# Kernel optimization log

Hardware: AMD Instinct MI355X
Metric: run time of the kernel (lower is better)

Reference implementation:

```python
import jax, jax.numpy as jnp
import numpy as np

N_E = 1024
E_DIM = 64
BETA = 0.25


def setup_inputs() -> dict:
    key = jax.random.key(0)
    k1, k2 = jax.random.split(key)
    z = jax.random.normal(k1, (16, E_DIM, 64, 64), dtype=jnp.float32)
    # embedding initialized uniform(-1/n_e, 1/n_e) as in the torch module
    emb = jax.random.uniform(k2, (N_E, E_DIM), dtype=jnp.float32,
                             minval=-1.0 / N_E, maxval=1.0 / N_E)
    return {"z": z, "emb": emb}


def reference(z, emb):
    n_e, e_dim = emb.shape
    # NCHW -> NHWC, flatten to tokens
    zp = jnp.transpose(z, (0, 2, 3, 1))            # [B,H,W,C]
    zf = zp.reshape(-1, e_dim)                      # [N,C]
    # squared distances ||zf||^2 + ||e||^2 - 2 zf e^T  -> [N, n_e]
    d = (jnp.sum(zf * zf, axis=1, keepdims=True)
         + jnp.sum(emb * emb, axis=1)
         - 2.0 * jnp.matmul(zf, emb.T))
    idx = jnp.argmin(d, axis=1)                     # [N]
    # one-hot @ emb is exactly a gather
    z_q = emb[idx].reshape(zp.shape)                # [B,H,W,C]
    loss = (jnp.mean((jax.lax.stop_gradient(z_q) - zp) ** 2)
            + BETA * jnp.mean((z_q - jax.lax.stop_gradient(zp)) ** 2))
    # straight-through estimator
    z_q = zp + jax.lax.stop_gradient(z_q - zp)
    # perplexity from codeword usage histogram
    counts = jax.ops.segment_sum(jnp.ones_like(idx, dtype=zf.dtype), idx,
                                 num_segments=n_e)
    e_mean = counts / zf.shape[0]
    perplexity = jnp.exp(-jnp.sum(e_mean * jnp.log(e_mean + 1e-10)))
    min_encoding_indices = idx.reshape(z.shape[0], -1).astype(jnp.int32)
    z_q = jnp.transpose(z_q, (0, 3, 1, 2))          # back to NCHW
    return z_q, loss, perplexity, min_encoding_indices
```

## Files before the change

### kernel.cpp

```cpp
#include <hip/hip_runtime.h>

#define TOKS 65536
#define ED 64
#define NE 1024
#define CH_STRIDE 4096
#define B_STRIDE 262144

typedef __bf16 bf16x8 __attribute__((ext_vector_type(8)));
typedef float f32x16 __attribute__((ext_vector_type(16)));
typedef unsigned short ushort_t;
typedef unsigned int uint_t;


__device__ __forceinline__ ushort_t f2bf(float x) {
    uint_t u = __float_as_uint(x);
    uint_t r = u + 0x7FFFu + ((u >> 16) & 1u);
    return (ushort_t)(r >> 16);
}

__global__ __launch_bounds__(256) void vq_prep_e(const float* __restrict__ emb,
                                                 ushort_t* __restrict__ efrag,
                                                 float* __restrict__ enorm,
                                                 int* __restrict__ hist,
                                                 double* __restrict__ lossAcc) {
    const int tid = threadIdx.x;
    const int w = tid >> 6, lane = tid & 63;
    const int j = blockIdx.x * 4 + w;

    const float e = emb[j * 64 + lane];
    const float sq = __fmul_rn(e, e);
    float acc = sq;
    acc = __fadd_rn(acc, __shfl_down(sq, 8, 64));
    acc = __fadd_rn(acc, __shfl_down(sq, 16, 64));
    acc = __fadd_rn(acc, __shfl_down(sq, 24, 64));
    acc = __fadd_rn(acc, __shfl_down(sq, 32, 64));
    acc = __fadd_rn(acc, __shfl_down(sq, 40, 64));
    acc = __fadd_rn(acc, __shfl_down(sq, 48, 64));
    acc = __fadd_rn(acc, __shfl_down(sq, 56, 64));
    float x = __fadd_rn(acc, __shfl_down(acc, 1, 64));
    float y = __fadd_rn(x, __shfl_down(x, 2, 64));
    float zn = __fadd_rn(y, __shfl_down(y, 4, 64));
    if (lane == 0) enorm[j] = zn;

    const ushort_t h = f2bf(-2.0f * e);
    const int ct = j >> 5, m = j & 31;
    const int ks = lane >> 4, kh = (lane >> 3) & 1, i = lane & 7;
    efrag[(size_t)((ct * 4 + ks) * 512) + (m + 32 * kh) * 8 + i] = h;

    if (blockIdx.x < 4) hist[blockIdx.x * 256 + tid] = 0;
    if (blockIdx.x == 0 && tid == 0) *lossAcc = 0.0;
}

__global__ __launch_bounds__(256, 4) void vq_main(
    const float* __restrict__ z,
    const ushort_t* __restrict__ efrag,
    const float* __restrict__ enorm,
    const float* __restrict__ emb,
    float* __restrict__ zq,
    float* __restrict__ out_idx,
    int* __restrict__ hist,
    double* __restrict__ lossAcc) {
    __shared__ float z_s[64][36];
    __shared__ uint_t skey[4][32][2][3];
    __shared__ float s_zn[32];
    __shared__ unsigned long long s_res[32];
    __shared__ uint_t s_cand[128];
    __shared__ int s_cnt;
    __shared__ double wsum[4];

    const int tid = threadIdx.x;
    const int w = tid >> 6, lane = tid & 63;
    const int t0 = blockIdx.x * 32;
    const int b = t0 >> 12, hw0 = t0 & 4095;
    const float* zbase = z + (size_t)b * B_STRIDE + hw0;

    {
        const int c = tid >> 2, u0 = (tid & 3) * 8;
        const float* src = zbase + (size_t)c * CH_STRIDE + u0;
        float4 f0 = *(const float4*)(src);
        float4 f1 = *(const float4*)(src + 4);
        *(float4*)&z_s[c][u0] = f0;
        *(float4*)&z_s[c][u0 + 4] = f1;
    }
    if (tid < 32) s_res[tid] = 0xFFFFFFFFFFFFFFFFull;
    if (tid == 0) s_cnt = 0;

    const int n = lane & 31, kh = lane >> 5;

    bf16x8 zb[4];
    #pragma unroll
    for (int ks = 0; ks < 4; ++ks) {
        #pragma unroll
        for (int i = 0; i < 8; ++i) {
            union { ushort_t u; __bf16 bh; } ca;
            ca.u = f2bf(zbase[(size_t)(ks * 16 + kh * 8 + i) * CH_STRIDE + n]);
            zb[ks][i] = ca.bh;
        }
    }

    uint_t k0 = 0xFFFFFFFFu, k1 = 0xFFFFFFFFu, k2 = 0xFFFFFFFFu;
    const bf16x8* eg = (const bf16x8*)efrag;

    #pragma unroll
    for (int ct = 0; ct < 8; ++ct) {
        const int gct = w * 8 + ct;
        bf16x8 ah0 = eg[(size_t)(gct * 4 + 0) * 64 + lane];
        bf16x8 ah1 = eg[(size_t)(gct * 4 + 1) * 64 + lane];
        bf16x8 ah2 = eg[(size_t)(gct * 4 + 2) * 64 + lane];
        bf16x8 ah3 = eg[(size_t)(gct * 4 + 3) * 64 + lane];

        f32x16 acc;
        #pragma unroll
        for (int r = 0; r < 16; ++r) acc[r] = 0.25f;
        acc = __builtin_amdgcn_mfma_f32_32x32x16_bf16(ah0, zb[0], acc, 0, 0, 0);
        acc = __builtin_amdgcn_mfma_f32_32x32x16_bf16(ah1, zb[1], acc, 0, 0, 0);
        acc = __builtin_amdgcn_mfma_f32_32x32x16_bf16(ah2, zb[2], acc, 0, 0, 0);
        acc = __builtin_amdgcn_mfma_f32_32x32x16_bf16(ah3, zb[3], acc, 0, 0, 0);

        const int jb = gct * 32 + 4 * kh;
        #pragma unroll
        for (int r = 0; r < 16; ++r) {
            uint_t key = (__float_as_uint(acc[r]) & 0xFFFFFC00u)
                         | (uint_t)(jb + (r & 3) + 8 * (r >> 2));
            uint_t mx = max(k0, key);
            k2 = min(k2, max(k1, mx));
            k1 = min(k1, mx);
            k0 = min(k0, key);
        }
    }

    skey[w][n][kh][0] = k0; skey[w][n][kh][1] = k1; skey[w][n][kh][2] = k2;
    __syncthreads();

    const int t_loc = tid >> 3, m = tid & 7;
    {
        float a = z_s[m][t_loc];
        float racc = __fmul_rn(a, a);
        #pragma unroll
        for (int i = 1; i < 8; ++i) {
            float av = z_s[m + 8 * i][t_loc];
            racc = __fadd_rn(racc, __fmul_rn(av, av));
        }
        float x1 = __fadd_rn(racc, __shfl_xor(racc, 1, 64));
        float y1 = __fadd_rn(x1, __shfl_xor(x1, 2, 64));
        float zn = __fadd_rn(y1, __shfl_xor(y1, 4, 64));
        if (m == 0) s_zn[t_loc] = zn;
    }
    {
        uint_t ck[3];
        #pragma unroll
        for (int s = 0; s < 3; ++s) ck[s] = skey[m >> 1][t_loc][m & 1][s];
        uint_t kmin = min(ck[0], min(ck[1], ck[2]));
        kmin = min(kmin, (uint_t)__shfl_xor((int)kmin, 1, 64));
        kmin = min(kmin, (uint_t)__shfl_xor((int)kmin, 2, 64));
        kmin = min(kmin, (uint_t)__shfl_xor((int)kmin, 4, 64));
        const float thr = __uint_as_float(kmin & 0xFFFFFC00u) + 4.0e-4f;
        #pragma unroll
        for (int s = 0; s < 3; ++s) {
            if (__uint_as_float(ck[s] & 0xFFFFFC00u) <= thr) {
                int pos = atomicAdd(&s_cnt, 1);
                if (pos < 128)
                    s_cand[pos] = ((uint_t)t_loc << 10) | (ck[s] & 1023u);
            }
        }
    }
    __syncthreads();

    {
        const int cnt = s_cnt;
        if (tid < cnt && tid < 128) {
            const uint_t cd = s_cand[tid];
            const int tok = (int)(cd >> 10), j = (int)(cd & 1023u);
            const float* e = emb + (size_t)j * 64;
            float a0 = 0.f;
            #pragma unroll
            for (int k4 = 0; k4 < 64; k4 += 4) {
                float4 e4 = *(const float4*)(e + k4);
                a0 = __fmaf_rn(z_s[k4 + 0][tok], e4.x, a0);
                a0 = __fmaf_rn(z_s[k4 + 1][tok], e4.y, a0);
                a0 = __fmaf_rn(z_s[k4 + 2][tok], e4.z, a0);
                a0 = __fmaf_rn(z_s[k4 + 3][tok], e4.w, a0);
            }
            float d = __fsub_rn(__fadd_rn(s_zn[tok], enorm[j]), 2.0f * a0);
            unsigned long long key =
                ((unsigned long long)__float_as_uint(d) << 10)
                | (unsigned long long)j;
            atomicMin(&s_res[tok], key);
        }
    }
    __syncthreads();

    const int bj = (int)(s_res[t_loc] & 1023u);
    if (m == 0) {
        out_idx[t0 + t_loc] = (float)bj;
        atomicAdd(&hist[bj], 1);
    }
    double ls = 0.0;
    {
        const float* e = emb + (size_t)bj * 64;
        #pragma unroll
        for (int i = 0; i < 8; ++i) {
            const int k = m + 8 * i;
            float ev = e[k];
            float zv = z_s[k][t_loc];
            z_s[k][t_loc] = ev;
            float df = ev - zv;
            ls += (double)(df * df);
        }
    }
    #pragma unroll
    for (int off = 32; off > 0; off >>= 1) ls += __shfl_down(ls, off, 64);
    if (lane == 0) wsum[w] = ls;
    __syncthreads();
    if (tid == 0)
        atomicAdd(lossAcc, wsum[0] + wsum[1] + wsum[2] + wsum[3]);

    {
        const int c = tid >> 2, u0 = (tid & 3) * 8;
        float4 f0 = *(const float4*)&z_s[c][u0];
        float4 f1 = *(const float4*)&z_s[c][u0 + 4];
        float* dst = zq + (size_t)b * B_STRIDE + (size_t)c * CH_STRIDE + hw0 + u0;
        *(float4*)(dst) = f0;
        *(float4*)(dst + 4) = f1;
    }
}

__global__ __launch_bounds__(256) void vq_final(const int* __restrict__ hist,
                                                const double* __restrict__ lossAcc,
                                                float* __restrict__ outs) {
    __shared__ double red[256];
    double acc = 0.0;
    for (int j = threadIdx.x; j < NE; j += 256) {
        double em = (double)hist[j] * (1.0 / 65536.0);
        acc += em * log(em + 1e-10);
    }
    red[threadIdx.x] = acc;
    __syncthreads();
    for (int s = 128; s > 0; s >>= 1) {
        if (threadIdx.x < s) red[threadIdx.x] += red[threadIdx.x + s];
        __syncthreads();
    }
    if (threadIdx.x == 0) {
        outs[0] = (float)(1.25 * (*lossAcc) * (1.0 / 4194304.0));
        outs[1] = (float)exp(-red[0]);
    }
}

extern "C" void kernel_launch(void* const* d_in, const int* in_sizes, int n_in,
                              void* d_out, int out_size, void* d_ws, size_t ws_size,
                              hipStream_t stream) {
    const float* z = (const float*)d_in[0];
    const float* emb = (const float*)d_in[1];
    float* out = (float*)d_out;

    char* ws = (char*)d_ws;
    ushort_t* efrag = (ushort_t*)ws;
    float* enorm = (float*)(ws + 131072);
    int* hist = (int*)(ws + 135168);
    double* lossAcc = (double*)(ws + 139264);

    float* zq = out;
    float* scalars = out + 4194304;
    float* out_idx = out + 4194306;

    vq_prep_e<<<256, 256, 0, stream>>>(emb, efrag, enorm, hist, lossAcc);
    vq_main<<<2048, 256, 0, stream>>>(z, efrag, enorm, emb, zq, out_idx, hist, lossAcc);
    vq_final<<<1, 256, 0, stream>>>(hist, lossAcc, scalars);
}
```

Before: 49.23 us.

## Replace top-3 key tracking with two-pass min-threshold candidate selection

The old code kept a sorted top-3 key per lane. The new code runs the MFMA distance tiles twice: the first pass finds only the per-token approximate minimum, and the second pass recomputes the tiles and collects every codeword within the threshold as a refinement candidate. The candidate buffer grows and occupancy hints drop to 2 blocks per CU. This removes the costly min/max insertion chain per element, and by collecting all near-ties it may avoid missing candidates that the top-3 scheme could drop. The price is double the MFMA work and double the efrag loads.

```diff
diff --git a/kernel.cpp b/kernel.cpp
--- a/kernel.cpp
+++ b/kernel.cpp
@@ -51,7 +51,7 @@
     if (blockIdx.x == 0 && tid == 0) *lossAcc = 0.0;
 }
 
-__global__ __launch_bounds__(256, 4) void vq_main(
+__global__ __launch_bounds__(256, 2) void vq_main(
     const float* __restrict__ z,
     const ushort_t* __restrict__ efrag,
     const float* __restrict__ enorm,
@@ -61,10 +61,10 @@
     int* __restrict__ hist,
     double* __restrict__ lossAcc) {
     __shared__ float z_s[64][36];
-    __shared__ uint_t skey[4][32][2][3];
+    __shared__ float smin[4][32];
     __shared__ float s_zn[32];
     __shared__ unsigned long long s_res[32];
-    __shared__ uint_t s_cand[128];
+    __shared__ uint_t s_cand[192];
     __shared__ int s_cnt;
     __shared__ double wsum[4];
 
@@ -98,9 +98,9 @@
         }
     }
 
-    uint_t k0 = 0xFFFFFFFFu, k1 = 0xFFFFFFFFu, k2 = 0xFFFFFFFFu;
     const bf16x8* eg = (const bf16x8*)efrag;
 
+    float vmin = 3.4e38f;
     #pragma unroll
     for (int ct = 0; ct < 8; ++ct) {
         const int gct = w * 8 + ct;
@@ -108,7 +108,6 @@
         bf16x8 ah1 = eg[(size_t)(gct * 4 + 1) * 64 + lane];
         bf16x8 ah2 = eg[(size_t)(gct * 4 + 2) * 64 + lane];
         bf16x8 ah3 = eg[(size_t)(gct * 4 + 3) * 64 + lane];
-
         f32x16 acc;
         #pragma unroll
         for (int r = 0; r < 16; ++r) acc[r] = 0.25f;
@@ -116,21 +115,15 @@
         acc = __builtin_amdgcn_mfma_f32_32x32x16_bf16(ah1, zb[1], acc, 0, 0, 0);
         acc = __builtin_amdgcn_mfma_f32_32x32x16_bf16(ah2, zb[2], acc, 0, 0, 0);
         acc = __builtin_amdgcn_mfma_f32_32x32x16_bf16(ah3, zb[3], acc, 0, 0, 0);
-
-        const int jb = gct * 32 + 4 * kh;
-        #pragma unroll
-        for (int r = 0; r < 16; ++r) {
-            uint_t key = (__float_as_uint(acc[r]) & 0xFFFFFC00u)
-                         | (uint_t)(jb + (r & 3) + 8 * (r >> 2));
-            uint_t mx = max(k0, key);
-            k2 = min(k2, max(k1, mx));
-            k1 = min(k1, mx);
-            k0 = min(k0, key);
-        }
-    }
-
-    skey[w][n][kh][0] = k0; skey[w][n][kh][1] = k1; skey[w][n][kh][2] = k2;
-    __syncthreads();
+        #pragma unroll
+        for (int r = 0; r < 16; ++r) vmin = fminf(vmin, acc[r]);
+    }
+    vmin = fminf(vmin, __shfl_xor(vmin, 32, 64));
+    if (kh == 0) smin[w][n] = vmin;
+    __syncthreads();
+
+    const float thr = fminf(fminf(smin[0][n], smin[1][n]),
+                            fminf(smin[2][n], smin[3][n])) + 4.0e-4f;
 
     const int t_loc = tid >> 3, m = tid & 7;
     {
@@ -146,21 +139,34 @@
         float zn = __fadd_rn(y1, __shfl_xor(y1, 4, 64));
         if (m == 0) s_zn[t_loc] = zn;
     }
-    {
-        uint_t ck[3];
-        #pragma unroll
-        for (int s = 0; s < 3; ++s) ck[s] = skey[m >> 1][t_loc][m & 1][s];
-        uint_t kmin = min(ck[0], min(ck[1], ck[2]));
-        kmin = min(kmin, (uint_t)__shfl_xor((int)kmin, 1, 64));
-        kmin = min(kmin, (uint_t)__shfl_xor((int)kmin, 2, 64));
-        kmin = min(kmin, (uint_t)__shfl_xor((int)kmin, 4, 64));
-        const float thr = __uint_as_float(kmin & 0xFFFFFC00u) + 4.0e-4f;
-        #pragma unroll
-        for (int s = 0; s < 3; ++s) {
-            if (__uint_as_float(ck[s] & 0xFFFFFC00u) <= thr) {
-                int pos = atomicAdd(&s_cnt, 1);
-                if (pos < 128)
-                    s_cand[pos] = ((uint_t)t_loc << 10) | (ck[s] & 1023u);
+
+    #pragma unroll
+    for (int ct = 0; ct < 8; ++ct) {
+        const int gct = w * 8 + ct;
+        bf16x8 ah0 = eg[(size_t)(gct * 4 + 0) * 64 + lane];
+        bf16x8 ah1 = eg[(size_t)(gct * 4 + 1) * 64 + lane];
+        bf16x8 ah2 = eg[(size_t)(gct * 4 + 2) * 64 + lane];
+        bf16x8 ah3 = eg[(size_t)(gct * 4 + 3) * 64 + lane];
+        f32x16 acc;
+        #pragma unroll
+        for (int r = 0; r < 16; ++r) acc[r] = 0.25f;
+        acc = __builtin_amdgcn_mfma_f32_32x32x16_bf16(ah0, zb[0], acc, 0, 0, 0);
+        acc = __builtin_amdgcn_mfma_f32_32x32x16_bf16(ah1, zb[1], acc, 0, 0, 0);
+        acc = __builtin_amdgcn_mfma_f32_32x32x16_bf16(ah2, zb[2], acc, 0, 0, 0);
+        acc = __builtin_amdgcn_mfma_f32_32x32x16_bf16(ah3, zb[3], acc, 0, 0, 0);
+        float m16 = acc[0];
+        #pragma unroll
+        for (int r = 1; r < 16; ++r) m16 = fminf(m16, acc[r]);
+        if (m16 <= thr) {
+            const int jb = gct * 32 + 4 * kh;
+            #pragma unroll
+            for (int r = 0; r < 16; ++r) {
+                if (acc[r] <= thr) {
+                    int pos = atomicAdd(&s_cnt, 1);
+                    if (pos < 192)
+                        s_cand[pos] = ((uint_t)n << 10)
+                                      | (uint_t)(jb + (r & 3) + 8 * (r >> 2));
+                }
             }
         }
     }
@@ -168,7 +174,7 @@
 
     {
         const int cnt = s_cnt;
-        if (tid < cnt && tid < 128) {
+        if (tid < cnt && tid < 192) {
             const uint_t cd = s_cand[tid];
             const int tok = (int)(cd >> 10), j = (int)(cd & 1023u);
             const float* e = emb + (size_t)j * 64;
```

Result: slower. 57.93 us (+17.7%).

## Process 64 tokens per block, reusing codebook fragments across two MFMA tiles

Applied to the files above, without the earlier changes.

Each block now handles 64 tokens instead of 32, running two token tiles against each loaded codebook fragment. This halves codebook fragment loads per token and halves the grid. Codebook fragments are software-prefetched one tile ahead, and per-lane candidate tracking drops from top-3 to top-2 per tile. The cost is higher register pressure and fewer, larger blocks. Top-2 tracking may also drop near-tie candidates that the exact rescoring previously caught.

```diff
diff --git a/kernel.cpp b/kernel.cpp
--- a/kernel.cpp
+++ b/kernel.cpp
@@ -60,115 +60,148 @@
     float* __restrict__ out_idx,
     int* __restrict__ hist,
     double* __restrict__ lossAcc) {
-    __shared__ float z_s[64][36];
-    __shared__ uint_t skey[4][32][2][3];
-    __shared__ float s_zn[32];
-    __shared__ unsigned long long s_res[32];
-    __shared__ uint_t s_cand[128];
+    __shared__ float z_s[64][68];
+    __shared__ uint_t skey[4][2][32][2][2];
+    __shared__ float s_zn[64];
+    __shared__ unsigned long long s_res[64];
+    __shared__ uint_t s_cand[256];
     __shared__ int s_cnt;
     __shared__ double wsum[4];
 
     const int tid = threadIdx.x;
     const int w = tid >> 6, lane = tid & 63;
-    const int t0 = blockIdx.x * 32;
+    const int t0 = blockIdx.x * 64;
     const int b = t0 >> 12, hw0 = t0 & 4095;
     const float* zbase = z + (size_t)b * B_STRIDE + hw0;
 
     {
-        const int c = tid >> 2, u0 = (tid & 3) * 8;
+        const int c = tid >> 2, u0 = (tid & 3) * 16;
         const float* src = zbase + (size_t)c * CH_STRIDE + u0;
         float4 f0 = *(const float4*)(src);
         float4 f1 = *(const float4*)(src + 4);
-        *(float4*)&z_s[c][u0] = f0;
-        *(float4*)&z_s[c][u0 + 4] = f1;
-    }
-    if (tid < 32) s_res[tid] = 0xFFFFFFFFFFFFFFFFull;
+        float4 f2 = *(const float4*)(src + 8);
+        float4 f3 = *(const float4*)(src + 12);
+        float4* dst = (float4*)&z_s[c][u0];
+        dst[0] = f0; dst[1] = f1; dst[2] = f2; dst[3] = f3;
+    }
+    if (tid < 64) s_res[tid] = 0xFFFFFFFFFFFFFFFFull;
     if (tid == 0) s_cnt = 0;
 
     const int n = lane & 31, kh = lane >> 5;
 
-    bf16x8 zb[4];
+    bf16x8 zbA[4], zbB[4];
     #pragma unroll
     for (int ks = 0; ks < 4; ++ks) {
         #pragma unroll
         for (int i = 0; i < 8; ++i) {
-            union { ushort_t u; __bf16 bh; } ca;
-            ca.u = f2bf(zbase[(size_t)(ks * 16 + kh * 8 + i) * CH_STRIDE + n]);
-            zb[ks][i] = ca.bh;
-        }
-    }
-
-    uint_t k0 = 0xFFFFFFFFu, k1 = 0xFFFFFFFFu, k2 = 0xFFFFFFFFu;
+            const size_t off = (size_t)(ks * 16 + kh * 8 + i) * CH_STRIDE;
+            union { ushort_t u; __bf16 bh; } ca, cb;
+            ca.u = f2bf(zbase[off + n]);
+            cb.u = f2bf(zbase[off + 32 + n]);
+            zbA[ks][i] = ca.bh;
+            zbB[ks][i] = cb.bh;
+        }
+    }
+
+    uint_t kA0 = 0xFFFFFFFFu, kA1 = 0xFFFFFFFFu;
+    uint_t kB0 = 0xFFFFFFFFu, kB1 = 0xFFFFFFFFu;
     const bf16x8* eg = (const bf16x8*)efrag;
 
-    #pragma unroll
+    bf16x8 ah0 = eg[(size_t)((w * 8) * 4 + 0) * 64 + lane];
+    bf16x8 ah1 = eg[(size_t)((w * 8) * 4 + 1) * 64 + lane];
+    bf16x8 ah2 = eg[(size_t)((w * 8) * 4 + 2) * 64 + lane];
+    bf16x8 ah3 = eg[(size_t)((w * 8) * 4 + 3) * 64 + lane];
+
     for (int ct = 0; ct < 8; ++ct) {
         const int gct = w * 8 + ct;
-        bf16x8 ah0 = eg[(size_t)(gct * 4 + 0) * 64 + lane];
-        bf16x8 ah1 = eg[(size_t)(gct * 4 + 1) * 64 + lane];
-        bf16x8 ah2 = eg[(size_t)(gct * 4 + 2) * 64 + lane];
-        bf16x8 ah3 = eg[(size_t)(gct * 4 + 3) * 64 + lane];
-
-        f32x16 acc;
-        #pragma unroll
-        for (int r = 0; r < 16; ++r) acc[r] = 0.25f;
-        acc = __builtin_amdgcn_mfma_f32_32x32x16_bf16(ah0, zb[0], acc, 0, 0, 0);
-        acc = __builtin_amdgcn_mfma_f32_32x32x16_bf16(ah1, zb[1], acc, 0, 0, 0);
-        acc = __builtin_amdgcn_mfma_f32_32x32x16_bf16(ah2, zb[2], acc, 0, 0, 0);
-        acc = __builtin_amdgcn_mfma_f32_32x32x16_bf16(ah3, zb[3], acc, 0, 0, 0);
-
+        bf16x8 nx0, nx1, nx2, nx3;
+        if (ct < 7) {
+            nx0 = eg[(size_t)((gct + 1) * 4 + 0) * 64 + lane];
+            nx1 = eg[(size_t)((gct + 1) * 4 + 1) * 64 + lane];
+            nx2 = eg[(size_t)((gct + 1) * 4 + 2) * 64 + lane];
+            nx3 = eg[(size_t)((gct + 1) * 4 + 3) * 64 + lane];
+        }
         const int jb = gct * 32 + 4 * kh;
+
+        f32x16 accA;
+        #pragma unroll
+        for (int r = 0; r < 16; ++r) accA[r] = 0.25f;
+        accA = __builtin_amdgcn_mfma_f32_32x32x16_bf16(ah0, zbA[0], accA, 0, 0, 0);
+        accA = __builtin_amdgcn_mfma_f32_32x32x16_bf16(ah1, zbA[1], accA, 0, 0, 0);
+        accA = __builtin_amdgcn_mfma_f32_32x32x16_bf16(ah2, zbA[2], accA, 0, 0, 0);
+        accA = __builtin_amdgcn_mfma_f32_32x32x16_bf16(ah3, zbA[3], accA, 0, 0, 0);
+
+        f32x16 accB;
+        #pragma unroll
+        for (int r = 0; r < 16; ++r) accB[r] = 0.25f;
+        accB = __builtin_amdgcn_mfma_f32_32x32x16_bf16(ah0, zbB[0], accB, 0, 0, 0);
+        accB = __builtin_amdgcn_mfma_f32_32x32x16_bf16(ah1, zbB[1], accB, 0, 0, 0);
+        accB = __builtin_amdgcn_mfma_f32_32x32x16_bf16(ah2, zbB[2], accB, 0, 0, 0);
+        accB = __builtin_amdgcn_mfma_f32_32x32x16_bf16(ah3, zbB[3], accB, 0, 0, 0);
+
         #pragma unroll
         for (int r = 0; r < 16; ++r) {
-            uint_t key = (__float_as_uint(acc[r]) & 0xFFFFFC00u)
-                         | (uint_t)(jb + (r & 3) + 8 * (r >> 2));
-            uint_t mx = max(k0, key);
-            k2 = min(k2, max(k1, mx));
-            k1 = min(k1, mx);
-            k0 = min(k0, key);
-        }
-    }
-
-    skey[w][n][kh][0] = k0; skey[w][n][kh][1] = k1; skey[w][n][kh][2] = k2;
-    __syncthreads();
-
-    const int t_loc = tid >> 3, m = tid & 7;
-    {
-        float a = z_s[m][t_loc];
-        float racc = __fmul_rn(a, a);
+            const uint_t jbits = (uint_t)(jb + (r & 3) + 8 * (r >> 2));
+            uint_t keyA = (__float_as_uint(accA[r]) & 0xFFFFFC00u) | jbits;
+            uint_t mxA = max(kA0, keyA);
+            kA1 = min(kA1, mxA);
+            kA0 = min(kA0, keyA);
+            uint_t keyB = (__float_as_uint(accB[r]) & 0xFFFFFC00u) | jbits;
+            uint_t mxB = max(kB0, keyB);
+            kB1 = min(kB1, mxB);
+            kB0 = min(kB0, keyB);
+        }
+        ah0 = nx0; ah1 = nx1; ah2 = nx2; ah3 = nx3;
+    }
+
+    skey[w][0][n][kh][0] = kA0; skey[w][0][n][kh][1] = kA1;
+    skey[w][1][n][kh][0] = kB0; skey[w][1][n][kh][1] = kB1;
+    __syncthreads();
+
+    const int t_loc = tid >> 2, m = tid & 3;
+    const int tile = t_loc >> 5, nn = t_loc & 31;
+    {
+        uint_t ck[4];
+        ck[0] = skey[m][tile][nn][0][0];
+        ck[1] = skey[m][tile][nn][0][1];
+        ck[2] = skey[m][tile][nn][1][0];
+        ck[3] = skey[m][tile][nn][1][1];
+        uint_t kmin = min(min(ck[0], ck[1]), min(ck[2], ck[3]));
+        kmin = min(kmin, (uint_t)__shfl_xor((int)kmin, 1, 64));
+        kmin = min(kmin, (uint_t)__shfl_xor((int)kmin, 2, 64));
+        const float thr = __uint_as_float(kmin & 0xFFFFFC00u) + 4.0e-4f;
+        #pragma unroll
+        for (int s = 0; s < 4; ++s) {
+            if (__uint_as_float(ck[s] & 0xFFFFFC00u) <= thr) {
+                int pos = atomicAdd(&s_cnt, 1);
+                if (pos < 256)
+                    s_cand[pos] = ((uint_t)t_loc << 10) | (ck[s] & 1023u);
+            }
+        }
+    }
+    {
+        float a0 = z_s[m][t_loc];
+        float ra = __fmul_rn(a0, a0);
+        float b0 = z_s[m + 4][t_loc];
+        float rb = __fmul_rn(b0, b0);
         #pragma unroll
         for (int i = 1; i < 8; ++i) {
             float av = z_s[m + 8 * i][t_loc];
-            racc = __fadd_rn(racc, __fmul_rn(av, av));
-        }
-        float x1 = __fadd_rn(racc, __shfl_xor(racc, 1, 64));
-        float y1 = __fadd_rn(x1, __shfl_xor(x1, 2, 64));
-        float zn = __fadd_rn(y1, __shfl_xor(y1, 4, 64));
-        if (m == 0) s_zn[t_loc] = zn;
-    }
-    {
-        uint_t ck[3];
-        #pragma unroll
-        for (int s = 0; s < 3; ++s) ck[s] = skey[m >> 1][t_loc][m & 1][s];
-        uint_t kmin = min(ck[0], min(ck[1], ck[2]));
-        kmin = min(kmin, (uint_t)__shfl_xor((int)kmin, 1, 64));
-        kmin = min(kmin, (uint_t)__shfl_xor((int)kmin, 2, 64));
-        kmin = min(kmin, (uint_t)__shfl_xor((int)kmin, 4, 64));
-        const float thr = __uint_as_float(kmin & 0xFFFFFC00u) + 4.0e-4f;
-        #pragma unroll
-        for (int s = 0; s < 3; ++s) {
-            if (__uint_as_float(ck[s] & 0xFFFFFC00u) <= thr) {
-                int pos = atomicAdd(&s_cnt, 1);
-                if (pos < 128)
-                    s_cand[pos] = ((uint_t)t_loc << 10) | (ck[s] & 1023u);
-            }
-        }
+            ra = __fadd_rn(ra, __fmul_rn(av, av));
+            float bv = z_s[m + 4 + 8 * i][t_loc];
+            rb = __fadd_rn(rb, __fmul_rn(bv, bv));
+        }
+        float xa = __fadd_rn(ra, __shfl_xor(ra, 1, 64));
+        float A = __fadd_rn(xa, __shfl_xor(xa, 2, 64));
+        float xb = __fadd_rn(rb, __shfl_xor(rb, 1, 64));
+        float B = __fadd_rn(xb, __shfl_xor(xb, 2, 64));
+        if (m == 0) s_zn[t_loc] = __fadd_rn(A, B);
     }
     __syncthreads();
 
     {
         const int cnt = s_cnt;
-        if (tid < cnt && tid < 128) {
+        if (tid < cnt && tid < 256) {
             const uint_t cd = s_cand[tid];
             const int tok = (int)(cd >> 10), j = (int)(cd & 1023u);
             const float* e = emb + (size_t)j * 64;
@@ -199,8 +232,8 @@
     {
         const float* e = emb + (size_t)bj * 64;
         #pragma unroll
-        for (int i = 0; i < 8; ++i) {
-            const int k = m + 8 * i;
+        for (int i = 0; i < 16; ++i) {
+            const int k = m + 4 * i;
             float ev = e[k];
             float zv = z_s[k][t_loc];
             z_s[k][t_loc] = ev;
@@ -216,12 +249,14 @@
         atomicAdd(lossAcc, wsum[0] + wsum[1] + wsum[2] + wsum[3]);
 
     {
-        const int c = tid >> 2, u0 = (tid & 3) * 8;
-        float4 f0 = *(const float4*)&z_s[c][u0];
-        float4 f1 = *(const float4*)&z_s[c][u0 + 4];
+        const int c = tid >> 2, u0 = (tid & 3) * 16;
+        const float4* s4 = (const float4*)&z_s[c][u0];
+        float4 f0 = s4[0], f1 = s4[1], f2 = s4[2], f3 = s4[3];
         float* dst = zq + (size_t)b * B_STRIDE + (size_t)c * CH_STRIDE + hw0 + u0;
         *(float4*)(dst) = f0;
         *(float4*)(dst + 4) = f1;
+        *(float4*)(dst + 8) = f2;
+        *(float4*)(dst + 12) = f3;
     }
 }
 
@@ -264,6 +299,6 @@
     float* out_idx = out + 4194306;
 
     vq_prep_e<<<256, 256, 0, stream>>>(emb, efrag, enorm, hist, lossAcc);
-    vq_main<<<2048, 256, 0, stream>>>(z, efrag, enorm, emb, zq, out_idx, hist, lossAcc);
+    vq_main<<<1024, 256, 0, stream>>>(z, efrag, enorm, emb, zq, out_idx, hist, lossAcc);
     vq_final<<<1, 256, 0, stream>>>(hist, lossAcc, scalars);
 }
```

After: 47.26 us. -4.0%, faster.

## Keep codebook fragments in registers and loop over token tiles with double-buffered staging

Applied to the files above, without the earlier changes.

The main kernel now uses 512-thread blocks, each handling 128 tokens in four 32-token tiles. Each wave loads its share of the bf16 codebook fragments into registers once and reuses them across all tiles, instead of reloading them per 32-token block. The next z tile is prefetched and staged into a double-buffered shared array, and the per-token refine step is done inline with two candidates per lane rather than an atomic candidate list. The global double atomic for the loss is replaced by per-block partial sums that the final kernel reduces. The cost is more registers, fewer blocks in flight, and more barriers per block.

```diff
diff --git a/kernel.cpp b/kernel.cpp
--- a/kernel.cpp
+++ b/kernel.cpp
@@ -21,8 +21,7 @@
 __global__ __launch_bounds__(256) void vq_prep_e(const float* __restrict__ emb,
                                                  ushort_t* __restrict__ efrag,
                                                  float* __restrict__ enorm,
-                                                 int* __restrict__ hist,
-                                                 double* __restrict__ lossAcc) {
+                                                 int* __restrict__ hist) {
     const int tid = threadIdx.x;
     const int w = tid >> 6, lane = tid & 63;
     const int j = blockIdx.x * 4 + w;
@@ -48,10 +47,9 @@
     efrag[(size_t)((ct * 4 + ks) * 512) + (m + 32 * kh) * 8 + i] = h;
 
     if (blockIdx.x < 4) hist[blockIdx.x * 256 + tid] = 0;
-    if (blockIdx.x == 0 && tid == 0) *lossAcc = 0.0;
-}
-
-__global__ __launch_bounds__(256, 4) void vq_main(
+}
+
+__global__ __launch_bounds__(512, 2) void vq_main(
     const float* __restrict__ z,
     const ushort_t* __restrict__ efrag,
     const float* __restrict__ enorm,
@@ -59,189 +57,204 @@
     float* __restrict__ zq,
     float* __restrict__ out_idx,
     int* __restrict__ hist,
-    double* __restrict__ lossAcc) {
-    __shared__ float z_s[64][36];
-    __shared__ uint_t skey[4][32][2][3];
-    __shared__ float s_zn[32];
+    double* __restrict__ lossPart) {
+    __shared__ float z_s[2][32][68];
+    __shared__ uint_t skey[8][32][2][2];
     __shared__ unsigned long long s_res[32];
-    __shared__ uint_t s_cand[128];
-    __shared__ int s_cnt;
-    __shared__ double wsum[4];
+    __shared__ double wsum[8];
 
     const int tid = threadIdx.x;
     const int w = tid >> 6, lane = tid & 63;
-    const int t0 = blockIdx.x * 32;
+    const int n = lane & 31, kh = lane >> 5;
+    const int t0 = blockIdx.x * 128;
     const int b = t0 >> 12, hw0 = t0 & 4095;
-    const float* zbase = z + (size_t)b * B_STRIDE + hw0;
-
-    {
-        const int c = tid >> 2, u0 = (tid & 3) * 8;
-        const float* src = zbase + (size_t)c * CH_STRIDE + u0;
-        float4 f0 = *(const float4*)(src);
-        float4 f1 = *(const float4*)(src + 4);
-        *(float4*)&z_s[c][u0] = f0;
-        *(float4*)&z_s[c][u0 + 4] = f1;
-    }
+    const float* zg = z + (size_t)b * B_STRIDE + hw0;
+
+    const bf16x8* eg = (const bf16x8*)efrag;
+    bf16x8 ef[4][4];
+    #pragma unroll
+    for (int ct = 0; ct < 4; ++ct)
+        #pragma unroll
+        for (int ks = 0; ks < 4; ++ks)
+            ef[ct][ks] = eg[(size_t)(((w * 4 + ct) * 4 + ks) * 64) + lane];
+
+    const int sc = tid >> 3, stk = (tid & 7) * 4;
+    const float* sbase = zg + (size_t)sc * CH_STRIDE + stk;
+
+    float4 sreg = *(const float4*)(sbase);
+    z_s[0][stk + 0][sc] = sreg.x; z_s[0][stk + 1][sc] = sreg.y;
+    z_s[0][stk + 2][sc] = sreg.z; z_s[0][stk + 3][sc] = sreg.w;
+    sreg = *(const float4*)(sbase + 32);
     if (tid < 32) s_res[tid] = 0xFFFFFFFFFFFFFFFFull;
-    if (tid == 0) s_cnt = 0;
-
-    const int n = lane & 31, kh = lane >> 5;
-
-    bf16x8 zb[4];
-    #pragma unroll
-    for (int ks = 0; ks < 4; ++ks) {
-        #pragma unroll
-        for (int i = 0; i < 8; ++i) {
-            union { ushort_t u; __bf16 bh; } ca;
-            ca.u = f2bf(zbase[(size_t)(ks * 16 + kh * 8 + i) * CH_STRIDE + n]);
-            zb[ks][i] = ca.bh;
-        }
-    }
-
-    uint_t k0 = 0xFFFFFFFFu, k1 = 0xFFFFFFFFu, k2 = 0xFFFFFFFFu;
-    const bf16x8* eg = (const bf16x8*)efrag;
-
-    #pragma unroll
-    for (int ct = 0; ct < 8; ++ct) {
-        const int gct = w * 8 + ct;
-        bf16x8 ah0 = eg[(size_t)(gct * 4 + 0) * 64 + lane];
-        bf16x8 ah1 = eg[(size_t)(gct * 4 + 1) * 64 + lane];
-        bf16x8 ah2 = eg[(size_t)(gct * 4 + 2) * 64 + lane];
-        bf16x8 ah3 = eg[(size_t)(gct * 4 + 3) * 64 + lane];
-
-        f32x16 acc;
-        #pragma unroll
-        for (int r = 0; r < 16; ++r) acc[r] = 0.25f;
-        acc = __builtin_amdgcn_mfma_f32_32x32x16_bf16(ah0, zb[0], acc, 0, 0, 0);
-        acc = __builtin_amdgcn_mfma_f32_32x32x16_bf16(ah1, zb[1], acc, 0, 0, 0);
-        acc = __builtin_amdgcn_mfma_f32_32x32x16_bf16(ah2, zb[2], acc, 0, 0, 0);
-        acc = __builtin_amdgcn_mfma_f32_32x32x16_bf16(ah3, zb[3], acc, 0, 0, 0);
-
-        const int jb = gct * 32 + 4 * kh;
-        #pragma unroll
-        for (int r = 0; r < 16; ++r) {
-            uint_t key = (__float_as_uint(acc[r]) & 0xFFFFFC00u)
-                         | (uint_t)(jb + (r & 3) + 8 * (r >> 2));
-            uint_t mx = max(k0, key);
-            k2 = min(k2, max(k1, mx));
-            k1 = min(k1, mx);
-            k0 = min(k0, key);
-        }
-    }
-
-    skey[w][n][kh][0] = k0; skey[w][n][kh][1] = k1; skey[w][n][kh][2] = k2;
     __syncthreads();
 
-    const int t_loc = tid >> 3, m = tid & 7;
-    {
-        float a = z_s[m][t_loc];
-        float racc = __fmul_rn(a, a);
-        #pragma unroll
-        for (int i = 1; i < 8; ++i) {
-            float av = z_s[m + 8 * i][t_loc];
-            racc = __fadd_rn(racc, __fmul_rn(av, av));
-        }
-        float x1 = __fadd_rn(racc, __shfl_xor(racc, 1, 64));
-        float y1 = __fadd_rn(x1, __shfl_xor(x1, 2, 64));
-        float zn = __fadd_rn(y1, __shfl_xor(y1, 4, 64));
-        if (m == 0) s_zn[t_loc] = zn;
-    }
-    {
-        uint_t ck[3];
-        #pragma unroll
-        for (int s = 0; s < 3; ++s) ck[s] = skey[m >> 1][t_loc][m & 1][s];
-        uint_t kmin = min(ck[0], min(ck[1], ck[2]));
+    double ls = 0.0;
+    uint_t jmask = 0xFFFFFC00u;
+    const int idbase = w * 128 + 4 * kh;
+
+    #pragma unroll 1
+    for (int t = 0; t < 4; ++t) {
+        const float* zs = &z_s[t & 1][0][0];
+        if (t < 3) {
+            float* zd = &z_s[(t + 1) & 1][0][0];
+            zd[(stk + 0) * 68 + sc] = sreg.x;
+            zd[(stk + 1) * 68 + sc] = sreg.y;
+            zd[(stk + 2) * 68 + sc] = sreg.z;
+            zd[(stk + 3) * 68 + sc] = sreg.w;
+        }
+        if (t < 2) sreg = *(const float4*)(sbase + (t + 2) * 32);
+
+        bf16x8 zb[4];
+        #pragma unroll
+        for (int ks = 0; ks < 4; ++ks) {
+            #pragma unroll
+            for (int i = 0; i < 8; ++i) {
+                union { ushort_t u; __bf16 bh; } cv;
+                cv.u = f2bf(zs[n * 68 + ks * 16 + kh * 8 + i]);
+                zb[ks][i] = cv.bh;
+            }
+        }
+
+        uint_t k0 = 0xFFFFFFFFu, k1 = 0xFFFFFFFFu;
+        #pragma unroll
+        for (int ct = 0; ct < 4; ++ct) {
+            f32x16 acc;
+            #pragma unroll
+            for (int r = 0; r < 16; ++r) acc[r] = 0.25f;
+            acc = __builtin_amdgcn_mfma_f32_32x32x16_bf16(ef[ct][0], zb[0], acc, 0, 0, 0);
+            acc = __builtin_amdgcn_mfma_f32_32x32x16_bf16(ef[ct][1], zb[1], acc, 0, 0, 0);
+            acc = __builtin_amdgcn_mfma_f32_32x32x16_bf16(ef[ct][2], zb[2], acc, 0, 0, 0);
+            acc = __builtin_amdgcn_mfma_f32_32x32x16_bf16(ef[ct][3], zb[3], acc, 0, 0, 0);
+            #pragma unroll
+            for (int r = 0; r < 16; ++r) {
+                uint_t key = (__float_as_uint(acc[r]) & jmask)
+                             | (uint_t)(idbase + ct * 32 + (r & 3) + 8 * (r >> 2));
+                uint_t mx = max(k0, key);
+                k1 = min(k1, mx);
+                k0 = min(k0, key);
+            }
+        }
+        skey[w][n][kh][0] = k0;
+        skey[w][n][kh][1] = k1;
+        __syncthreads();
+
+        const int tok = tid >> 4, p = tid & 15;
+        const int tg = t0 + t * 32 + tok;
+        uint_t ck0 = skey[p >> 1][tok][p & 1][0];
+        uint_t ck1 = skey[p >> 1][tok][p & 1][1];
+        uint_t kmin = min(ck0, ck1);
         kmin = min(kmin, (uint_t)__shfl_xor((int)kmin, 1, 64));
         kmin = min(kmin, (uint_t)__shfl_xor((int)kmin, 2, 64));
         kmin = min(kmin, (uint_t)__shfl_xor((int)kmin, 4, 64));
-        const float thr = __uint_as_float(kmin & 0xFFFFFC00u) + 4.0e-4f;
-        #pragma unroll
-        for (int s = 0; s < 3; ++s) {
-            if (__uint_as_float(ck[s] & 0xFFFFFC00u) <= thr) {
-                int pos = atomicAdd(&s_cnt, 1);
-                if (pos < 128)
-                    s_cand[pos] = ((uint_t)t_loc << 10) | (ck[s] & 1023u);
-            }
-        }
-    }
-    __syncthreads();
-
-    {
-        const int cnt = s_cnt;
-        if (tid < cnt && tid < 128) {
-            const uint_t cd = s_cand[tid];
-            const int tok = (int)(cd >> 10), j = (int)(cd & 1023u);
-            const float* e = emb + (size_t)j * 64;
-            float a0 = 0.f;
-            #pragma unroll
-            for (int k4 = 0; k4 < 64; k4 += 4) {
-                float4 e4 = *(const float4*)(e + k4);
-                a0 = __fmaf_rn(z_s[k4 + 0][tok], e4.x, a0);
-                a0 = __fmaf_rn(z_s[k4 + 1][tok], e4.y, a0);
-                a0 = __fmaf_rn(z_s[k4 + 2][tok], e4.z, a0);
-                a0 = __fmaf_rn(z_s[k4 + 3][tok], e4.w, a0);
-            }
-            float d = __fsub_rn(__fadd_rn(s_zn[tok], enorm[j]), 2.0f * a0);
-            unsigned long long key =
-                ((unsigned long long)__float_as_uint(d) << 10)
-                | (unsigned long long)j;
-            atomicMin(&s_res[tok], key);
-        }
-    }
-    __syncthreads();
-
-    const int bj = (int)(s_res[t_loc] & 1023u);
-    if (m == 0) {
-        out_idx[t0 + t_loc] = (float)bj;
-        atomicAdd(&hist[bj], 1);
-    }
-    double ls = 0.0;
-    {
-        const float* e = emb + (size_t)bj * 64;
-        #pragma unroll
-        for (int i = 0; i < 8; ++i) {
-            const int k = m + 8 * i;
-            float ev = e[k];
-            float zv = z_s[k][t_loc];
-            z_s[k][t_loc] = ev;
-            float df = ev - zv;
-            ls += (double)(df * df);
-        }
-    }
+        kmin = min(kmin, (uint_t)__shfl_xor((int)kmin, 8, 64));
+        const float thr = __uint_as_float(kmin & jmask) + 4.0e-4f;
+
+        float zn;
+        {
+            const int m = p & 7;
+            float a = zs[tok * 68 + m];
+            float racc = __fmul_rn(a, a);
+            #pragma unroll
+            for (int i = 1; i < 8; ++i) {
+                float av = zs[tok * 68 + m + 8 * i];
+                racc = __fadd_rn(racc, __fmul_rn(av, av));
+            }
+            float x1 = __fadd_rn(racc, __shfl_xor(racc, 1, 64));
+            float y1 = __fadd_rn(x1, __shfl_xor(x1, 2, 64));
+            zn = __fadd_rn(y1, __shfl_xor(y1, 4, 64));
+        }
+
+        #pragma unroll
+        for (int s = 0; s < 2; ++s) {
+            const uint_t ck = s ? ck1 : ck0;
+            if (__uint_as_float(ck & jmask) <= thr) {
+                const int j = (int)(ck & 1023u);
+                const float* e = emb + (size_t)j * 64;
+                float a0 = 0.f;
+                #pragma unroll
+                for (int k4 = 0; k4 < 16; ++k4) {
+                    float4 z4 = *(const float4*)&zs[tok * 68 + k4 * 4];
+                    float4 e4 = *(const float4*)(e + k4 * 4);
+                    a0 = __fmaf_rn(z4.x, e4.x, a0);
+                    a0 = __fmaf_rn(z4.y, e4.y, a0);
+                    a0 = __fmaf_rn(z4.z, e4.z, a0);
+                    a0 = __fmaf_rn(z4.w, e4.w, a0);
+                }
+                float d = __fsub_rn(__fadd_rn(zn, enorm[j]), 2.0f * a0);
+                unsigned long long key =
+                    ((unsigned long long)__float_as_uint(d) << 10)
+                    | (unsigned long long)j;
+                atomicMin(&s_res[tok], key);
+            }
+        }
+        __syncthreads();
+
+        const int bj = (int)(s_res[tok] & 1023u);
+        if (p == 0) {
+            out_idx[tg] = (float)bj;
+            atomicAdd(&hist[bj], 1);
+        }
+        {
+            float4 e4 = *(const float4*)(emb + (size_t)bj * 64 + p * 4);
+            float* zrow = (float*)&z_s[t & 1][tok][p * 4];
+            float df;
+            df = e4.x - zrow[0]; ls += (double)(df * df);
+            df = e4.y - zrow[1]; ls += (double)(df * df);
+            df = e4.z - zrow[2]; ls += (double)(df * df);
+            df = e4.w - zrow[3]; ls += (double)(df * df);
+            zrow[0] = e4.x; zrow[1] = e4.y; zrow[2] = e4.z; zrow[3] = e4.w;
+        }
+        __syncthreads();
+
+        {
+            float4 f;
+            f.x = z_s[t & 1][stk + 0][sc];
+            f.y = z_s[t & 1][stk + 1][sc];
+            f.z = z_s[t & 1][stk + 2][sc];
+            f.w = z_s[t & 1][stk + 3][sc];
+            *(float4*)(zq + (size_t)b * B_STRIDE + (size_t)sc * CH_STRIDE
+                       + hw0 + t * 32 + stk) = f;
+        }
+        if (tid < 32) s_res[tid] = 0xFFFFFFFFFFFFFFFFull;
+        __syncthreads();
+    }
+
     #pragma unroll
     for (int off = 32; off > 0; off >>= 1) ls += __shfl_down(ls, off, 64);
     if (lane == 0) wsum[w] = ls;
     __syncthreads();
-    if (tid == 0)
-        atomicAdd(lossAcc, wsum[0] + wsum[1] + wsum[2] + wsum[3]);
-
-    {
-        const int c = tid >> 2, u0 = (tid & 3) * 8;
-        float4 f0 = *(const float4*)&z_s[c][u0];
-        float4 f1 = *(const float4*)&z_s[c][u0 + 4];
-        float* dst = zq + (size_t)b * B_STRIDE + (size_t)c * CH_STRIDE + hw0 + u0;
-        *(float4*)(dst) = f0;
-        *(float4*)(dst + 4) = f1;
+    if (tid == 0) {
+        double tot = 0.0;
+        #pragma unroll
+        for (int i = 0; i < 8; ++i) tot += wsum[i];
+        lossPart[blockIdx.x] = tot;
     }
 }
 
 __global__ __launch_bounds__(256) void vq_final(const int* __restrict__ hist,
-                                                const double* __restrict__ lossAcc,
+                                                const double* __restrict__ lossPart,
                                                 float* __restrict__ outs) {
     __shared__ double red[256];
+    __shared__ double red2[256];
     double acc = 0.0;
     for (int j = threadIdx.x; j < NE; j += 256) {
         double em = (double)hist[j] * (1.0 / 65536.0);
         acc += em * log(em + 1e-10);
     }
+    double lsum = 0.0;
+    for (int j = threadIdx.x; j < 512; j += 256) lsum += lossPart[j];
     red[threadIdx.x] = acc;
+    red2[threadIdx.x] = lsum;
     __syncthreads();
     for (int s = 128; s > 0; s >>= 1) {
-        if (threadIdx.x < s) red[threadIdx.x] += red[threadIdx.x + s];
+        if (threadIdx.x < s) {
+            red[threadIdx.x] += red[threadIdx.x + s];
+            red2[threadIdx.x] += red2[threadIdx.x + s];
+        }
         __syncthreads();
     }
     if (threadIdx.x == 0) {
-        outs[0] = (float)(1.25 * (*lossAcc) * (1.0 / 4194304.0));
+        outs[0] = (float)(1.25 * red2[0] * (1.0 / 4194304.0));
         outs[1] = (float)exp(-red[0]);
     }
 }
@@ -257,13 +270,14 @@
     ushort_t* efrag = (ushort_t*)ws;
     float* enorm = (float*)(ws + 131072);
     int* hist = (int*)(ws + 135168);
-    double* lossAcc = (double*)(ws + 139264);
+    double* lossPart = (double*)(ws + 143360);
 
     float* zq = out;
     float* scalars = out + 4194304;
     float* out_idx = out + 4194306;
 
-    vq_prep_e<<<256, 256, 0, stream>>>(emb, efrag, enorm, hist, lossAcc);
-    vq_main<<<2048, 256, 0, stream>>>(z, efrag, enorm, emb, zq, out_idx, hist, lossAcc);
-    vq_final<<<1, 256, 0, stream>>>(hist, lossAcc, scalars);
-}
+    vq_prep_e<<<256, 256, 0, stream>>>(emb, efrag, enorm, hist);
+    vq_main<<<512, 512, 0, stream>>>(z, efrag, enorm, emb, zq, out_idx,
+                                     hist, lossPart);
+    vq_final<<<1, 256, 0, stream>>>(hist, lossPart, scalars);
+}
```

Result: slower. 56.96 us (+15.7%).
